# Optimization experiments

Hardware: AMD Instinct MI355X
Metric: run time of the kernel (lower is better)

The kernel has to match this reference:

```python
import jax, jax.numpy as jnp
import numpy as np

# --- module hyperparameters (init_kwargs) ---
IN_CH = 512
OUT_CH = 512
NUM_HEADS = 8
MODES = 64
LQ = 4096
LKV = 4096
E = IN_CH // NUM_HEADS      # per-head input dim = 64
EO = OUT_CH // NUM_HEADS    # per-head output dim = 64
B = 16

# mode_select_method='lowest' -> lowest-frequency modes, sorted (deterministic)
INDEX_Q = np.arange(min(MODES, LQ // 2))    # [Mq]
INDEX_KV = np.arange(min(MODES, LKV // 2))  # [Mkv]
SCALE = 1.0 / (IN_CH * OUT_CH)


def setup_inputs() -> dict:
    key = jax.random.key(0)
    kq, kk, kv, kw1, kw2 = jax.random.split(key, 5)
    return {
        "q": jax.random.normal(kq, (B, LQ, NUM_HEADS, E), jnp.float32),
        "k": jax.random.normal(kk, (B, LKV, NUM_HEADS, E), jnp.float32),
        "v": jax.random.normal(kv, (B, LKV, NUM_HEADS, E), jnp.float32),
        "weights1": SCALE * jax.random.normal(kw1, (NUM_HEADS, E, EO, len(INDEX_Q)), jnp.float32),
        "weights2": SCALE * jax.random.normal(kw2, (NUM_HEADS, E, EO, len(INDEX_Q)), jnp.float32),
    }


def reference(q, k, v, weights1, weights2):
    # q: [B, Lq, H, E]; k, v: [B, Lkv, H, E] (v is computed-but-unused in the
    # original forward; kept for signature fidelity).
    Bq, Lq, H, _ = q.shape
    xq = jnp.transpose(q, (0, 2, 3, 1))  # [B, H, E, Lq]
    xk = jnp.transpose(k, (0, 2, 3, 1))  # [B, H, E, Lkv]

    # rFFT along time, then gather the selected frequency modes
    xq_ft = jnp.fft.rfft(xq, axis=-1)[..., INDEX_Q]    # [B, H, E, Mq] complex
    xk_ft = jnp.fft.rfft(xk, axis=-1)[..., INDEX_KV]   # [B, H, E, Mkv] complex

    # complex cross-attention over modes (contract head-dim E)
    xqk = jnp.einsum('bhex,bhey->bhxy', xq_ft, xk_ft)  # [B, H, Mq, Mkv]
    # tanh applied independently to real/imag parts (as in compl activation)
    xqk = jax.lax.complex(jnp.tanh(xqk.real), jnp.tanh(xqk.imag))

    xqkv = jnp.einsum('bhxy,bhey->bhex', xqk, xk_ft)   # [B, H, E, Mq]

    w = jax.lax.complex(weights1, weights2)            # [H, E, EO, Mq]
    xqkvw = jnp.einsum('bhex,heox->bhox', xqkv, w)     # [B, H, EO, Mq]

    # scatter selected modes back into full half-spectrum, inverse FFT
    out_ft = jnp.zeros((Bq, H, EO, Lq // 2 + 1), jnp.complex64)
    out_ft = out_ft.at[..., INDEX_Q].set(xqkvw)
    out = jnp.fft.irfft(out_ft, n=Lq, axis=-1)         # [B, H, EO, Lq]

    out = jnp.transpose(out, (0, 3, 1, 2)) / (IN_CH * OUT_CH)  # [B, Lq, H, EO]
    return out
```

## Files before the change

kernel.cpp:

```cpp
#include <hip/hip_runtime.h>
#include <math.h>


constexpr float TWOPI_L = 1.5339807878856412e-3f;

typedef __attribute__((ext_vector_type(8))) short short8;
typedef __attribute__((ext_vector_type(4))) float f32x4;

__device__ __forceinline__ unsigned short f2bf(float f) {
    unsigned int u = __builtin_bit_cast(unsigned int, f);
    unsigned int r = (u + 0x7fffu + ((u >> 16) & 1u)) >> 16;
    return (unsigned short)r;
}
__device__ __forceinline__ float bf2f(unsigned short h) {
    unsigned int u = ((unsigned int)h) << 16;
    return __builtin_bit_cast(float, u);
}
__device__ __forceinline__ unsigned int cvtpk(float a, float b) {
    unsigned int r;
    asm("v_cvt_pk_bf16_f32 %0, %1, %2" : "=v"(r) : "v"(a), "v"(b));
    return r;
}
__device__ __forceinline__ void gld16(const float* g, void* l) {
    __builtin_amdgcn_global_load_lds(
        (const __attribute__((address_space(1))) void*)(g),
        (__attribute__((address_space(3))) void*)(l),
        16, 0, 0);
}
#define MSKR(r) (((((r) & 7)) << 1) | ((((r) >> 3)) & 1))

__global__ __launch_bounds__(256) void k0_twiddle(unsigned short* __restrict__ Whi,
                                                  unsigned short* __restrict__ Wlo) {
    const int idx = blockIdx.x * 256 + threadIdx.x;
    const int kt = idx >> 9;
    const int rb = (idx >> 6) & 7;
    const int l15 = (idx >> 2) & 15;
    const int lg = idx & 3;
    const int r_tab = rb * 16 + l15;
    int m, c;
    if (r_tab < 64) { m = (r_tab >> 1) * 2;              c = r_tab & 1; }
    else            { m = (((r_tab - 64) >> 1) * 2) + 1; c = r_tab & 1; }
    const int addr = (kt * 8 + rb) * 512 + l15 * 32 + lg * 8;
    unsigned short hbuf[8], lbuf[8];
#pragma unroll
    for (int j = 0; j < 8; ++j) {
        const int t = kt * 32 + lg * 8 + j;
        float sv, cv;
        sincosf((float)((m * t) & 4095) * TWOPI_L, &sv, &cv);
        const float v = c ? -sv : cv;
        const unsigned short hi = f2bf(v);
        hbuf[j] = hi;
        lbuf[j] = f2bf(v - bf2f(hi));
    }
    *(uint4*)(Whi + addr) = *(uint4*)hbuf;
    *(uint4*)(Wlo + addr) = *(uint4*)lbuf;
}

__global__ __launch_bounds__(256) void k0_basis(unsigned short* __restrict__ basis) {
    const int idx = blockIdx.x * 256 + threadIdx.x;
    const int p0 = idx << 2;
    const int t = p0 >> 6;
    unsigned int pk[4];
#pragma unroll
    for (int j = 0; j < 4; ++j) {
        const int m = (p0 & 63) + j;
        float sv, cv;
        sincosf((float)((m * t) & 4095) * TWOPI_L, &sv, &cv);
        const float c = (m == 0) ? 1.0f : 2.0f * cv;
        const float s = (m == 0) ? 0.0f : -2.0f * sv;
        pk[j] = (unsigned int)f2bf(c) | ((unsigned int)f2bf(s) << 16);
    }
    *(uint4*)(basis + (size_t)t * 128u + ((p0 & 63) << 1)) =
        make_uint4(pk[0], pk[1], pk[2], pk[3]);
}

__global__ __launch_bounds__(256, 3) void k1_mfma(const float* __restrict__ q,
                                                  const float* __restrict__ kin,
                                                  const unsigned short* __restrict__ Whi,
                                                  const unsigned short* __restrict__ Wlo,
                                                  float* __restrict__ Xq, float* __restrict__ Xk,
                                                  float* __restrict__ Pq, float* __restrict__ Pk)
{
    __shared__ float raw[2][64][64];
    __shared__ unsigned short xT[4][64][40];

    const int tid = threadIdx.x;
    const int bid = blockIdx.x;
    const int bh = bid >> 3, src = (bid >> 2) & 1, seg = bid & 3;
    const int b = bh >> 3, h = bh & 7;
    const float* __restrict__ x = src ? kin : q;
    const float* xb = x + (size_t)b * 2097152u + (size_t)h * 64u;

    const int wid = tid >> 6, lane = tid & 63;
    const int l15 = lane & 15, lg = lane >> 4;
    const int fp = (tid & 15) * 2;
    const int eqs = tid >> 4;
    const int sel = (wid >> 1) * 2;

    f32x4 acc[2][4];
#pragma unroll
    for (int mt = 0; mt < 2; ++mt)
#pragma unroll
        for (int nt = 0; nt < 4; ++nt)
            acc[mt][nt] = (f32x4){0.f, 0.f, 0.f, 0.f};

#define K1_STAGE(IT, NXT) do {                                                  \
    const int t0_ = (seg * 16 + (IT)) * 32;                                     \
    _Pragma("unroll")                                                           \
    for (int j = 0; j < 4; ++j) {                                               \
        const int c_ = wid * 4 + j;                                             \
        const int rl_ = 4 * c_ + (lane >> 4);                                   \
        const int t_ = t0_ + (rl_ & 31) + ((rl_ >> 5) << 11);                   \
        const int sq_ = (lane & 15) ^ MSKR(rl_);                                \
        gld16(xb + (size_t)t_ * 512u + (size_t)(sq_ * 4), &raw[NXT][c_ * 4][0]); \
    }                                                                           \
} while (0)

#define K1_TILE(IT, CUR, STAGE_STMT, VMC) do {                                  \
    short8 Ah[2], Al[2];                                                        \
    const int ksg_ = seg * 16 + (IT);                                           \
    _Pragma("unroll")                                                           \
    for (int mt = 0; mt < 2; ++mt) {                                            \
        const size_t o_ = (size_t)((ksg_ * 8 + (wid * 2 + mt)) * 512 + l15 * 32 + lg * 8); \
        Ah[mt] = *(const short8*)(Whi + o_);                                    \
        Al[mt] = *(const short8*)(Wlo + o_);                                    \
    }                                                                           \
    __builtin_amdgcn_sched_barrier(0);    \
    STAGE_STMT;                                                                 \
    asm volatile("s_waitcnt vmcnt(" #VMC ")\n\ts_barrier" ::: "memory");        \
    {           \
        float rs[16];                                                           \
        *(f32x4*)&rs[0]  = *(const f32x4*)&raw[CUR][fp     ][(eqs ^ MSKR(fp))      * 4]; \
        *(f32x4*)&rs[4]  = *(const f32x4*)&raw[CUR][fp + 1 ][(eqs ^ MSKR(fp + 1))  * 4]; \
        *(f32x4*)&rs[8]  = *(const f32x4*)&raw[CUR][fp + 32][(eqs ^ MSKR(fp + 32)) * 4]; \
        *(f32x4*)&rs[12] = *(const f32x4*)&raw[CUR][fp + 33][(eqs ^ MSKR(fp + 33)) * 4]; \
        _Pragma("unroll")                                                       \
        for (int ee = 0; ee < 4; ++ee) {                                        \
            const float a0 = rs[ee], a1 = rs[4 + ee];                           \
            const float c0 = rs[8 + ee], c1 = rs[12 + ee];                      \
            const float xp0 = a0 + c0, xp1 = a1 + c1;                           \
            const float xm0 = a0 - c0, xm1 = a1 - c1;                           \
            const int e_ = eqs * 4 + ee;                                        \
            const unsigned int php = cvtpk(xp0, xp1);                           \
            const float ph0 = __builtin_bit_cast(float, php << 16);             \
            const float ph1 = __builtin_bit_cast(float, php & 0xffff0000u);     \
            const unsigned int plp = cvtpk(xp0 - ph0, xp1 - ph1);               \
            const unsigned int mhp = cvtpk(xm0, xm1);                           \
            const float mh0 = __builtin_bit_cast(float, mhp << 16);             \
            const float mh1 = __builtin_bit_cast(float, mhp & 0xffff0000u);     \
            const unsigned int mlp = cvtpk(xm0 - mh0, xm1 - mh1);               \
            *(unsigned int*)&xT[0][e_][fp] = php;                               \
            *(unsigned int*)&xT[1][e_][fp] = plp;                               \
            *(unsigned int*)&xT[2][e_][fp] = mhp;                               \
            *(unsigned int*)&xT[3][e_][fp] = mlp;                               \
        }                                                                       \
    }                                                                           \
    asm volatile("s_waitcnt lgkmcnt(0)\n\ts_barrier" ::: "memory");             \
    {             \
        const unsigned short* sh = &xT[sel][0][0];                              \
        const unsigned short* sl = &xT[sel + 1][0][0];                          \
        _Pragma("unroll")                                                       \
        for (int nt = 0; nt < 4; ++nt) {                                        \
            const int ri = (nt * 16 + l15) * 40 + 8 * lg;                       \
            const short8 Bh = *(const short8*)(sh + ri);                        \
            const short8 Bl = *(const short8*)(sl + ri);                        \
            _Pragma("unroll")                                                   \
            for (int mt = 0; mt < 2; ++mt)                                      \
                acc[mt][nt] = __builtin_amdgcn_mfma_f32_16x16x32_bf16(Ah[mt], Bh, acc[mt][nt], 0, 0, 0); \
            _Pragma("unroll")                                                   \
            for (int mt = 0; mt < 2; ++mt)                                      \
                acc[mt][nt] = __builtin_amdgcn_mfma_f32_16x16x32_bf16(Ah[mt], Bl, acc[mt][nt], 0, 0, 0); \
            _Pragma("unroll")                                                   \
            for (int mt = 0; mt < 2; ++mt)                                      \
                acc[mt][nt] = __builtin_amdgcn_mfma_f32_16x16x32_bf16(Al[mt], Bh, acc[mt][nt], 0, 0, 0); \
        }                                                                       \
    }                                                                           \
} while (0)

    K1_STAGE(0, 0);
    for (int it = 0; it < 15; ++it) {
        K1_TILE(it, (it & 1), K1_STAGE(it + 1, (it + 1) & 1), 8);
    }
    K1_TILE(15, 1, (void)0, 4);

#undef K1_TILE
#undef K1_STAGE

    float* Xd;
    if (seg == 0) Xd = src ? Xk : Xq;
    else          Xd = (src ? Pk : Pq) + (size_t)(seg - 1) * 1048576u;
    Xd += (size_t)bh * 8192u;
    const int oddw = wid >> 1;
    const int wb = wid & 1;
#pragma unroll
    for (int mt = 0; mt < 2; ++mt) {
        const int r0 = (wb * 2 + mt) * 32 + 8 * lg + 2 * oddw;
#pragma unroll
        for (int nt = 0; nt < 4; ++nt) {
            const int e = nt * 16 + l15;
            *(float2*)(Xd + (size_t)e * 128u + r0) =
                make_float2(acc[mt][nt][0], acc[mt][nt][1]);
            *(float2*)(Xd + (size_t)e * 128u + r0 + 4) =
                make_float2(acc[mt][nt][2], acc[mt][nt][3]);
        }
    }
}

__global__ __launch_bounds__(256) void k1_reduce(float* __restrict__ Xq, const float* __restrict__ Pq,
                                                 float* __restrict__ Xk, const float* __restrict__ Pk) {
    const int i = blockIdx.x * 256 + threadIdx.x;
    float4* a = (float4*)Xq;
    float4* c = (float4*)Xk;
    float4 v = a[i], w = c[i];
#pragma unroll
    for (int s = 0; s < 3; ++s) {
        const float4 p = ((const float4*)(Pq + (size_t)s * 1048576u))[i];
        const float4 r = ((const float4*)(Pk + (size_t)s * 1048576u))[i];
        v.x += p.x; v.y += p.y; v.z += p.z; v.w += p.w;
        w.x += r.x; w.y += r.y; w.z += r.z; w.w += r.w;
    }
    a[i] = v;
    c[i] = w;
}

__global__ __launch_bounds__(256) void k2a_p1(const float* __restrict__ Xq,
                                              const float* __restrict__ Xk,
                                              float* __restrict__ P)
{
    const int blk = blockIdx.x;
    const int bh = blk >> 2, xt = blk & 3;
    __shared__ float sQ[64 * 32];
    __shared__ float sK[64 * 128];
    const int tid = threadIdx.x;
    const float* Xqb = Xq + (size_t)bh * 8192u;
    const float* Xkb = Xk + (size_t)bh * 8192u;

#pragma unroll
    for (int p = 0; p < 2; ++p) {
        const int f4 = tid + p * 256;
        const int row = f4 >> 3, c4 = f4 & 7;
        *(float4*)&sQ[row * 32 + c4 * 4] = *(const float4*)(Xqb + row * 128 + xt * 32 + c4 * 4);
    }
#pragma unroll
    for (int p = 0; p < 8; ++p) {
        const int f4 = tid + p * 256;
        *(float4*)&sK[f4 * 4] = *(const float4*)(Xkb + f4 * 4);
    }
    __syncthreads();

    const int xg = tid & 15, yg = tid >> 4;
    float aR[4] = {0.f, 0.f, 0.f, 0.f}, aI[4] = {0.f, 0.f, 0.f, 0.f};
#pragma unroll 8
    for (int e = 0; e < 64; ++e) {
        const float2 qv = *(const float2*)&sQ[e * 32 + 2 * xg];
        const float4 k0 = *(const float4*)&sK[e * 128 + 8 * yg];
        const float4 k1v = *(const float4*)&sK[e * 128 + 8 * yg + 4];
        aR[0] += qv.x * k0.x - qv.y * k0.y;   aI[0] += qv.x * k0.y + qv.y * k0.x;
        aR[1] += qv.x * k0.z - qv.y * k0.w;   aI[1] += qv.x * k0.w + qv.y * k0.z;
        aR[2] += qv.x * k1v.x - qv.y * k1v.y; aI[2] += qv.x * k1v.y + qv.y * k1v.x;
        aR[3] += qv.x * k1v.z - qv.y * k1v.w; aI[3] += qv.x * k1v.w + qv.y * k1v.z;
    }
    float* Pb = P + (size_t)bh * 8192u;
    const int x_abs = xt * 16 + xg;
#pragma unroll
    for (int j = 0; j < 4; ++j) {
        const int y = 4 * yg + j;
        *(float2*)(Pb + (size_t)y * 128u + 2 * x_abs) =
            make_float2(tanhf(aR[j]), tanhf(aI[j]));
    }
}

__global__ __launch_bounds__(256) void k2b_p3(const float* __restrict__ P,
                                              const float* __restrict__ Xk,
                                              float* __restrict__ PVG)
{
    const int blk = blockIdx.x;
    const int bh = blk >> 2, et = blk & 3;
    const int b = bh >> 3, h = bh & 7;
    __shared__ float sP[64 * 128];
    __shared__ float sKe[16 * 132];
    const int tid = threadIdx.x;
    const float* Pb = P + (size_t)bh * 8192u;
    const float* Xkb = Xk + (size_t)bh * 8192u + (size_t)(et * 16) * 128u;

#pragma unroll
    for (int p = 0; p < 8; ++p) {
        const int f4 = tid + p * 256;
        *(float4*)&sP[f4 * 4] = *(const float4*)(Pb + f4 * 4);
    }
#pragma unroll
    for (int p = 0; p < 2; ++p) {
        const int f4 = tid + p * 256;
        const int row = f4 >> 5, c4 = f4 & 31;
        *(float4*)&sKe[row * 132 + c4 * 4] = *(const float4*)(Xkb + row * 128 + c4 * 4);
    }
    __syncthreads();

    const int xg = tid & 15, el = tid >> 4;
    float aR[4] = {0.f, 0.f, 0.f, 0.f}, aI[4] = {0.f, 0.f, 0.f, 0.f};
#pragma unroll 8
    for (int y = 0; y < 64; ++y) {
        const float2 kv = *(const float2*)&sKe[el * 132 + 2 * y];
        const float4 p0 = *(const float4*)&sP[y * 128 + 8 * xg];
        const float4 p1 = *(const float4*)&sP[y * 128 + 8 * xg + 4];
        aR[0] += p0.x * kv.x - p0.y * kv.y;   aI[0] += p0.x * kv.y + p0.y * kv.x;
        aR[1] += p0.z * kv.x - p0.w * kv.y;   aI[1] += p0.z * kv.y + p0.w * kv.x;
        aR[2] += p1.x * kv.x - p1.y * kv.y;   aI[2] += p1.x * kv.y + p1.y * kv.x;
        aR[3] += p1.z * kv.x - p1.w * kv.y;   aI[3] += p1.z * kv.y + p1.w * kv.x;
    }
    const int e_abs = et * 16 + el;
    float* base = PVG + (size_t)h * 131072u;
#pragma unroll
    for (int j = 0; j < 4; ++j) {
        const int m = 4 * xg + j;
        base[(size_t)m * 2048u + 0u    + (size_t)b * 64u + e_abs] = aR[j];
        base[(size_t)m * 2048u + 1024u + (size_t)b * 64u + e_abs] = aI[j];
    }
}

__global__ __launch_bounds__(256) void kwt(const float* __restrict__ w1,
                                           const float* __restrict__ w2,
                                           float* __restrict__ wT)
{
    const int blk = blockIdx.x;
    const int h = blk >> 6, e = blk & 63;
    const int tid = threadIdx.x;
    const int m = tid & 63, oq = tid >> 6;
    const float* w1b = w1 + ((size_t)(h * 64 + e)) * 4096u;
    const float* w2b = w2 + ((size_t)(h * 64 + e)) * 4096u;
    float buf[32];
#pragma unroll
    for (int i = 0; i < 16; ++i) {
        const int o = oq * 16 + i;
        buf[2 * i]     = w1b[o * 64 + m];
        buf[2 * i + 1] = w2b[o * 64 + m];
    }
    float* dst = wT + (((size_t)(h * 64 + m)) * 64u + e) * 128u + oq * 32;
#pragma unroll
    for (int i = 0; i < 8; ++i)
        *(float4*)(dst + i * 4) = *(float4*)&buf[i * 4];
}

__global__ __launch_bounds__(256) void k2c_p4(const float* __restrict__ PVG,
                                              const float* __restrict__ wT,
                                              unsigned short* __restrict__ XWThi,
                                              unsigned short* __restrict__ XWTlo)
{
    const int blk = blockIdx.x;
    const int h = blk >> 6, m = blk & 63;
    __shared__ float sA[32 * 68];
    __shared__ float sW[64 * 128];
    const int tid = threadIdx.x;
    const float* Ab = PVG + (size_t)h * 131072u + (size_t)m * 2048u;
    const float* Wb = wT + ((size_t)h * 64u + m) * 8192u;

#pragma unroll
    for (int p = 0; p < 2; ++p) {
        const int f4 = tid + p * 256;
        const int row = f4 >> 4, e0 = (f4 & 15) * 4;
        *(float4*)&sA[row * 68 + e0] = *(const float4*)(Ab + row * 64 + e0);
    }
#pragma unroll
    for (int p = 0; p < 8; ++p) {
        const int f4 = tid + p * 256;
        *(float4*)&sW[f4 * 4] = *(const float4*)(Wb + f4 * 4);
    }
    __syncthreads();

    const int og = tid & 15, b = tid >> 4;
    float aR[4] = {0.f, 0.f, 0.f, 0.f}, aI[4] = {0.f, 0.f, 0.f, 0.f};
#pragma unroll 8
    for (int e = 0; e < 64; ++e) {
        const float pR = sA[b * 68 + e];
        const float pI = sA[(16 + b) * 68 + e];
        const float4 w0 = *(const float4*)&sW[e * 128 + 8 * og];
        const float4 w1v = *(const float4*)&sW[e * 128 + 8 * og + 4];
        aR[0] += pR * w0.x - pI * w0.y;   aI[0] += pR * w0.y + pI * w0.x;
        aR[1] += pR * w0.z - pI * w0.w;   aI[1] += pR * w0.w + pI * w0.z;
        aR[2] += pR * w1v.x - pI * w1v.y; aI[2] += pR * w1v.y + pI * w1v.x;
        aR[3] += pR * w1v.z - pI * w1v.w; aI[3] += pR * w1v.w + pI * w1v.z;
    }
    const int bh = b * 8 + h;
    unsigned short* Th = XWThi + (size_t)bh * 8192u;
    unsigned short* Tl = XWTlo + (size_t)bh * 8192u;
#pragma unroll
    for (int j = 0; j < 4; ++j) {
        const int o = 4 * og + j;
        const unsigned int hp = cvtpk(aR[j], aI[j]);
        const float hR = __builtin_bit_cast(float, hp << 16);
        const float hI = __builtin_bit_cast(float, hp & 0xffff0000u);
        const unsigned int lp = cvtpk(aR[j] - hR, aI[j] - hI);
        *(unsigned int*)(Th + (size_t)o * 128u + 2 * m) = hp;
        *(unsigned int*)(Tl + (size_t)o * 128u + 2 * m) = lp;
    }
}

__global__ __launch_bounds__(256, 3) void k3_mfma(const unsigned short* __restrict__ basis,
                                                  const unsigned short* __restrict__ XWThi,
                                                  const unsigned short* __restrict__ XWTlo,
                                                  float* __restrict__ out)
{
    const int bid = blockIdx.x;
    const int bh = bid >> 4, tc = bid & 15;
    const int b = bh >> 3, h = bh & 7;
    const int tid = threadIdx.x;
    const int wid = tid >> 6, lane = tid & 63;
    const int l15 = lane & 15, lg = lane >> 4;

    const int t0 = tc * 256 + wid * 64;
    const unsigned short* Th = XWThi + (size_t)bh * 8192u;
    const unsigned short* Tl = XWTlo + (size_t)bh * 8192u;

    f32x4 acc[4][4];
#pragma unroll
    for (int mt = 0; mt < 4; ++mt)
#pragma unroll
        for (int nt = 0; nt < 4; ++nt)
            acc[mt][nt] = (f32x4){0.f, 0.f, 0.f, 0.f};

#pragma unroll
    for (int ks = 0; ks < 4; ++ks) {
        const int ko = ks * 32 + 8 * lg;
        short8 A[4], Bh[4], Bl[4];
#pragma unroll
        for (int mt = 0; mt < 4; ++mt)
            A[mt] = *(const short8*)(basis + (size_t)(t0 + mt * 16 + l15) * 128u + ko);
#pragma unroll
        for (int nt = 0; nt < 4; ++nt) {
            Bh[nt] = *(const short8*)(Th + (size_t)(nt * 16 + l15) * 128u + ko);
            Bl[nt] = *(const short8*)(Tl + (size_t)(nt * 16 + l15) * 128u + ko);
        }
#pragma unroll
        for (int mt = 0; mt < 4; ++mt)
#pragma unroll
            for (int nt = 0; nt < 4; ++nt)
                acc[mt][nt] = __builtin_amdgcn_mfma_f32_16x16x32_bf16(A[mt], Bh[nt], acc[mt][nt], 0, 0, 0);
#pragma unroll
        for (int mt = 0; mt < 4; ++mt)
#pragma unroll
            for (int nt = 0; nt < 4; ++nt)
                acc[mt][nt] = __builtin_amdgcn_mfma_f32_16x16x32_bf16(A[mt], Bl[nt], acc[mt][nt], 0, 0, 0);
    }

    const float scale = 9.313225746154785e-10f;
#pragma unroll
    for (int mt = 0; mt < 4; ++mt)
#pragma unroll
        for (int nt = 0; nt < 4; ++nt) {
            const int o = nt * 16 + l15;
#pragma unroll
            for (int j = 0; j < 4; ++j) {
                const int t = t0 + mt * 16 + 4 * lg + j;
                out[((size_t)(b * 4096 + t) * 8u + (size_t)h) * 64u + o] = acc[mt][nt][j] * scale;
            }
        }
}

extern "C" void kernel_launch(void* const* d_in, const int* in_sizes, int n_in,
                              void* d_out, int out_size, void* d_ws, size_t ws_size,
                              hipStream_t stream) {
    (void)in_sizes; (void)n_in; (void)out_size; (void)ws_size;
    const float* q  = (const float*)d_in[0];
    const float* k  = (const float*)d_in[1];
    const float* w1 = (const float*)d_in[3];
    const float* w2 = (const float*)d_in[4];
    float* out = (float*)d_out;

    float* ws = (float*)d_ws;
    float* Xq = ws;
    float* Xk = ws + 1048576;
    unsigned short* XWThi = (unsigned short*)(ws + 2097152);
    unsigned short* XWTlo = XWThi + 1048576;
    unsigned short* basis = (unsigned short*)ws;

    unsigned short* Whi = (unsigned short*)out;
    unsigned short* Wlo = Whi + 262144;
    float* Pq  = out + 524288;
    float* Pk  = out + 3670016;
    float* P   = out + 16777216;
    float* wT  = out + 17825792;
    float* PVG = out + 22020096;

    hipLaunchKernelGGL(k0_twiddle, dim3(128),  dim3(256), 0, stream, Whi, Wlo);
    hipLaunchKernelGGL(k1_mfma,    dim3(1024), dim3(256), 0, stream, q, k, Whi, Wlo, Xq, Xk, Pq, Pk);
    hipLaunchKernelGGL(k1_reduce,  dim3(1024), dim3(256), 0, stream, Xq, Pq, Xk, Pk);
    hipLaunchKernelGGL(k2a_p1,     dim3(512),  dim3(256), 0, stream, Xq, Xk, P);
    hipLaunchKernelGGL(k0_basis,   dim3(256),  dim3(256), 0, stream, basis);
    hipLaunchKernelGGL(k2b_p3,     dim3(512),  dim3(256), 0, stream, P, Xk, PVG);
    hipLaunchKernelGGL(kwt,        dim3(512),  dim3(256), 0, stream, w1, w2, wT);
    hipLaunchKernelGGL(k2c_p4,     dim3(512),  dim3(256), 0, stream, PVG, wT, XWThi, XWTlo);
    hipLaunchKernelGGL(k3_mfma,    dim3(2048), dim3(256), 0, stream, basis, XWThi, XWTlo, out);
}
```

Baseline: 213.1 us.

## Triple-buffer k1 input staging with prefetch distance two and LDS-transpose weight kernel

```diff
diff --git a/kernel.cpp b/kernel.cpp
--- a/kernel.cpp
+++ b/kernel.cpp
@@ -74,14 +74,14 @@
         make_uint4(pk[0], pk[1], pk[2], pk[3]);
 }
 
-__global__ __launch_bounds__(256, 3) void k1_mfma(const float* __restrict__ q,
+__global__ __launch_bounds__(256, 2) void k1_mfma(const float* __restrict__ q,
                                                   const float* __restrict__ kin,
                                                   const unsigned short* __restrict__ Whi,
                                                   const unsigned short* __restrict__ Wlo,
                                                   float* __restrict__ Xq, float* __restrict__ Xk,
                                                   float* __restrict__ Pq, float* __restrict__ Pk)
 {
-    __shared__ float raw[2][64][64];
+    __shared__ float raw[3][64][64];
     __shared__ unsigned short xT[4][64][40];
 
     const int tid = threadIdx.x;
@@ -104,86 +104,107 @@
         for (int nt = 0; nt < 4; ++nt)
             acc[mt][nt] = (f32x4){0.f, 0.f, 0.f, 0.f};
 
-#define K1_STAGE(IT, NXT) do {                                                  \
-    const int t0_ = (seg * 16 + (IT)) * 32;                                     \
+#define K1_STAGE(IT, BUF) do {                                                  \
+    const int t0_ = (seg * 16 + ((IT) & 15)) * 32;                              \
+    float* rbase_ = &raw[BUF][0][0];                                            \
     _Pragma("unroll")                                                           \
     for (int j = 0; j < 4; ++j) {                                               \
         const int c_ = wid * 4 + j;                                             \
         const int rl_ = 4 * c_ + (lane >> 4);                                   \
         const int t_ = t0_ + (rl_ & 31) + ((rl_ >> 5) << 11);                   \
         const int sq_ = (lane & 15) ^ MSKR(rl_);                                \
-        gld16(xb + (size_t)t_ * 512u + (size_t)(sq_ * 4), &raw[NXT][c_ * 4][0]); \
+        gld16(xb + (size_t)t_ * 512u + (size_t)(sq_ * 4), rbase_ + c_ * 256);   \
     }                                                                           \
 } while (0)
 
-#define K1_TILE(IT, CUR, STAGE_STMT, VMC) do {                                  \
-    short8 Ah[2], Al[2];                                                        \
-    const int ksg_ = seg * 16 + (IT);                                           \
+#define K1_ALOAD(IT, AH, AL) do {                                               \
+    const int ksg_ = seg * 16 + ((IT) & 15);                                    \
     _Pragma("unroll")                                                           \
     for (int mt = 0; mt < 2; ++mt) {                                            \
         const size_t o_ = (size_t)((ksg_ * 8 + (wid * 2 + mt)) * 512 + l15 * 32 + lg * 8); \
-        Ah[mt] = *(const short8*)(Whi + o_);                                    \
-        Al[mt] = *(const short8*)(Wlo + o_);                                    \
-    }                                                                           \
-    __builtin_amdgcn_sched_barrier(0);    \
-    STAGE_STMT;                                                                 \
-    asm volatile("s_waitcnt vmcnt(" #VMC ")\n\ts_barrier" ::: "memory");        \
-    {           \
-        float rs[16];                                                           \
-        *(f32x4*)&rs[0]  = *(const f32x4*)&raw[CUR][fp     ][(eqs ^ MSKR(fp))      * 4]; \
-        *(f32x4*)&rs[4]  = *(const f32x4*)&raw[CUR][fp + 1 ][(eqs ^ MSKR(fp + 1))  * 4]; \
-        *(f32x4*)&rs[8]  = *(const f32x4*)&raw[CUR][fp + 32][(eqs ^ MSKR(fp + 32)) * 4]; \
-        *(f32x4*)&rs[12] = *(const f32x4*)&raw[CUR][fp + 33][(eqs ^ MSKR(fp + 33)) * 4]; \
-        _Pragma("unroll")                                                       \
-        for (int ee = 0; ee < 4; ++ee) {                                        \
-            const float a0 = rs[ee], a1 = rs[4 + ee];                           \
-            const float c0 = rs[8 + ee], c1 = rs[12 + ee];                      \
-            const float xp0 = a0 + c0, xp1 = a1 + c1;                           \
-            const float xm0 = a0 - c0, xm1 = a1 - c1;                           \
-            const int e_ = eqs * 4 + ee;                                        \
-            const unsigned int php = cvtpk(xp0, xp1);                           \
-            const float ph0 = __builtin_bit_cast(float, php << 16);             \
-            const float ph1 = __builtin_bit_cast(float, php & 0xffff0000u);     \
-            const unsigned int plp = cvtpk(xp0 - ph0, xp1 - ph1);               \
-            const unsigned int mhp = cvtpk(xm0, xm1);                           \
-            const float mh0 = __builtin_bit_cast(float, mhp << 16);             \
-            const float mh1 = __builtin_bit_cast(float, mhp & 0xffff0000u);     \
-            const unsigned int mlp = cvtpk(xm0 - mh0, xm1 - mh1);               \
-            *(unsigned int*)&xT[0][e_][fp] = php;                               \
-            *(unsigned int*)&xT[1][e_][fp] = plp;                               \
-            *(unsigned int*)&xT[2][e_][fp] = mhp;                               \
-            *(unsigned int*)&xT[3][e_][fp] = mlp;                               \
-        }                                                                       \
-    }                                                                           \
-    asm volatile("s_waitcnt lgkmcnt(0)\n\ts_barrier" ::: "memory");             \
-    {             \
-        const unsigned short* sh = &xT[sel][0][0];                              \
-        const unsigned short* sl = &xT[sel + 1][0][0];                          \
-        _Pragma("unroll")                                                       \
-        for (int nt = 0; nt < 4; ++nt) {                                        \
-            const int ri = (nt * 16 + l15) * 40 + 8 * lg;                       \
-            const short8 Bh = *(const short8*)(sh + ri);                        \
-            const short8 Bl = *(const short8*)(sl + ri);                        \
-            _Pragma("unroll")                                                   \
-            for (int mt = 0; mt < 2; ++mt)                                      \
-                acc[mt][nt] = __builtin_amdgcn_mfma_f32_16x16x32_bf16(Ah[mt], Bh, acc[mt][nt], 0, 0, 0); \
-            _Pragma("unroll")                                                   \
-            for (int mt = 0; mt < 2; ++mt)                                      \
-                acc[mt][nt] = __builtin_amdgcn_mfma_f32_16x16x32_bf16(Ah[mt], Bl, acc[mt][nt], 0, 0, 0); \
-            _Pragma("unroll")                                                   \
-            for (int mt = 0; mt < 2; ++mt)                                      \
-                acc[mt][nt] = __builtin_amdgcn_mfma_f32_16x16x32_bf16(Al[mt], Bh, acc[mt][nt], 0, 0, 0); \
-        }                                                                       \
+        AH[mt] = *(const short8*)(Whi + o_);                                    \
+        AL[mt] = *(const short8*)(Wlo + o_);                                    \
     }                                                                           \
 } while (0)
 
+#define K1_CONVERT(BUF) do {                                                    \
+    const float* rb_ = &raw[BUF][0][0];                                         \
+    float rs[16];                                                               \
+    *(f32x4*)&rs[0]  = *(const f32x4*)(rb_ + (fp     ) * 64 + ((eqs ^ MSKR(fp))      * 4)); \
+    *(f32x4*)&rs[4]  = *(const f32x4*)(rb_ + (fp + 1 ) * 64 + ((eqs ^ MSKR(fp + 1))  * 4)); \
+    *(f32x4*)&rs[8]  = *(const f32x4*)(rb_ + (fp + 32) * 64 + ((eqs ^ MSKR(fp + 32)) * 4)); \
+    *(f32x4*)&rs[12] = *(const f32x4*)(rb_ + (fp + 33) * 64 + ((eqs ^ MSKR(fp + 33)) * 4)); \
+    _Pragma("unroll")                                                           \
+    for (int ee = 0; ee < 4; ++ee) {                                            \
+        const float a0 = rs[ee], a1 = rs[4 + ee];                               \
+        const float c0 = rs[8 + ee], c1 = rs[12 + ee];                          \
+        const float xp0 = a0 + c0, xp1 = a1 + c1;                               \
+        const float xm0 = a0 - c0, xm1 = a1 - c1;                               \
+        const int e_ = eqs * 4 + ee;                                            \
+        const unsigned int php = cvtpk(xp0, xp1);                               \
+        const float ph0 = __builtin_bit_cast(float, php << 16);                 \
+        const float ph1 = __builtin_bit_cast(float, php & 0xffff0000u);         \
+        const unsigned int plp = cvtpk(xp0 - ph0, xp1 - ph1);                   \
+        const unsigned int mhp = cvtpk(xm0, xm1);                               \
+        const float mh0 = __builtin_bit_cast(float, mhp << 16);                 \
+        const float mh1 = __builtin_bit_cast(float, mhp & 0xffff0000u);         \
+        const unsigned int mlp = cvtpk(xm0 - mh0, xm1 - mh1);                   \
+        *(unsigned int*)&xT[0][e_][fp] = php;                                   \
+        *(unsigned int*)&xT[1][e_][fp] = plp;                                   \
+        *(unsigned int*)&xT[2][e_][fp] = mhp;                                   \
+        *(unsigned int*)&xT[3][e_][fp] = mlp;                                   \
+    }                                                                           \
+} while (0)
+
+#define K1_MFMA(AH, AL) do {                                                    \
+    const unsigned short* sh = &xT[sel][0][0];                                  \
+    const unsigned short* sl = &xT[sel + 1][0][0];                              \
+    _Pragma("unroll")                                                           \
+    for (int nt = 0; nt < 4; ++nt) {                                            \
+        const int ri = (nt * 16 + l15) * 40 + 8 * lg;                           \
+        const short8 Bh = *(const short8*)(sh + ri);                            \
+        const short8 Bl = *(const short8*)(sl + ri);                            \
+        _Pragma("unroll")                                                       \
+        for (int mt = 0; mt < 2; ++mt)                                          \
+            acc[mt][nt] = __builtin_amdgcn_mfma_f32_16x16x32_bf16(AH[mt], Bh, acc[mt][nt], 0, 0, 0); \
+        _Pragma("unroll")                                                       \
+        for (int mt = 0; mt < 2; ++mt)                                          \
+            acc[mt][nt] = __builtin_amdgcn_mfma_f32_16x16x32_bf16(AH[mt], Bl, acc[mt][nt], 0, 0, 0); \
+        _Pragma("unroll")                                                       \
+        for (int mt = 0; mt < 2; ++mt)                                          \
+            acc[mt][nt] = __builtin_amdgcn_mfma_f32_16x16x32_bf16(AL[mt], Bh, acc[mt][nt], 0, 0, 0); \
+    }                                                                           \
+} while (0)
+
+    short8 AhA[2], AlA[2], AhB[2], AlB[2];
     K1_STAGE(0, 0);
-    for (int it = 0; it < 15; ++it) {
-        K1_TILE(it, (it & 1), K1_STAGE(it + 1, (it + 1) & 1), 8);
-    }
-    K1_TILE(15, 1, (void)0, 4);
-
-#undef K1_TILE
+    K1_ALOAD(0, AhA, AlA);
+    K1_STAGE(1, 1);
+
+    for (int itp = 0; itp < 8; ++itp) {
+        const int it0 = 2 * itp;
+        const int be = it0 % 3, bo = (it0 + 1) % 3;
+        const int bs1 = (it0 + 2) % 3, bs2 = (it0 + 3) % 3;
+        K1_ALOAD(it0 + 1, AhB, AlB);
+        K1_STAGE(it0 + 2, bs1);
+        __builtin_amdgcn_sched_barrier(0);
+        asm volatile("s_waitcnt vmcnt(12)\n\ts_barrier" ::: "memory");
+        K1_CONVERT(be);
+        asm volatile("s_waitcnt lgkmcnt(0)\n\ts_barrier" ::: "memory");
+        K1_MFMA(AhA, AlA);
+        K1_ALOAD(it0 + 2, AhA, AlA);
+        K1_STAGE(it0 + 3, bs2);
+        __builtin_amdgcn_sched_barrier(0);
+        asm volatile("s_waitcnt vmcnt(12)\n\ts_barrier" ::: "memory");
+        K1_CONVERT(bo);
+        asm volatile("s_waitcnt lgkmcnt(0)\n\ts_barrier" ::: "memory");
+        K1_MFMA(AhB, AlB);
+    }
+    asm volatile("s_waitcnt vmcnt(0)" ::: "memory");
+
+#undef K1_MFMA
+#undef K1_CONVERT
+#undef K1_ALOAD
 #undef K1_STAGE
 
     float* Xd;
@@ -324,21 +345,28 @@
 {
     const int blk = blockIdx.x;
     const int h = blk >> 6, e = blk & 63;
+    __shared__ float s1[64][65];
+    __shared__ float s2[64][65];
     const int tid = threadIdx.x;
-    const int m = tid & 63, oq = tid >> 6;
-    const float* w1b = w1 + ((size_t)(h * 64 + e)) * 4096u;
-    const float* w2b = w2 + ((size_t)(h * 64 + e)) * 4096u;
-    float buf[32];
-#pragma unroll
-    for (int i = 0; i < 16; ++i) {
-        const int o = oq * 16 + i;
-        buf[2 * i]     = w1b[o * 64 + m];
-        buf[2 * i + 1] = w2b[o * 64 + m];
-    }
-    float* dst = wT + (((size_t)(h * 64 + m)) * 64u + e) * 128u + oq * 32;
-#pragma unroll
-    for (int i = 0; i < 8; ++i)
-        *(float4*)(dst + i * 4) = *(float4*)&buf[i * 4];
+    const float* w1b = w1 + (size_t)(h * 64 + e) * 4096u;
+    const float* w2b = w2 + (size_t)(h * 64 + e) * 4096u;
+#pragma unroll
+    for (int p = 0; p < 4; ++p) {
+        const int f4 = tid + p * 256;
+        const int o = f4 >> 4, m4 = (f4 & 15) * 4;
+        *(float4*)&s1[o][m4] = *(const float4*)(w1b + f4 * 4);
+        *(float4*)&s2[o][m4] = *(const float4*)(w2b + f4 * 4);
+    }
+    __syncthreads();
+    float* dstb = wT + ((size_t)(h * 64) * 64u + (size_t)e) * 128u;
+#pragma unroll
+    for (int p = 0; p < 8; ++p) {
+        const int f4 = tid + p * 256;
+        const int m = f4 >> 5, c4 = f4 & 31;
+        const int o = c4 * 2;
+        const float4 v = make_float4(s1[o][m], s2[o][m], s1[o + 1][m], s2[o + 1][m]);
+        *(float4*)(dstb + (size_t)m * 8192u + c4 * 4) = v;
+    }
 }
 
 __global__ __launch_bounds__(256) void k2c_p4(const float* __restrict__ PVG,
```

Result: faster. 206.4 us (-3.2%).
